# Kernel optimization log

Hardware: AMD Instinct MI355X
Metric: run time of the kernel (lower is better)

Reference implementation:

```python
import jax, jax.numpy as jnp
import numpy as np

DN = ('NCHW', 'OIHW', 'NCHW')


def setup_inputs() -> dict:
    key = jax.random.key(0)
    k1, k2, k3, k4 = jax.random.split(key, 4)
    B, C, H, W = 8, 64, 128, 416
    depth = jax.random.uniform(k1, (B, H, W), dtype=jnp.float32) * 10.0 + 1.0
    feat = jax.random.normal(k2, (B, C, H, W), dtype=jnp.float32)
    w1 = jax.random.normal(k3, (64, C, 3, 3), dtype=jnp.float32) * 0.05
    w2 = jax.random.normal(k4, (144, 64, 1, 1), dtype=jnp.float32) * 0.05
    return {"depth": depth, "feat": feat, "w1": w1, "w2": w2}


def reference(depth, feat, w1, w2):
    B, H, W = depth.shape
    S = 4  # 2 ** scale, scale=2
    # mask predictor: conv3x3 (no bias) -> relu -> conv1x1 (no bias)
    h = jax.lax.conv_general_dilated(feat, w1, (1, 1), ((1, 1), (1, 1)), dimension_numbers=DN)
    h = jax.nn.relu(h)
    mask = jax.lax.conv_general_dilated(h, w2, (1, 1), ((0, 0), (0, 0)), dimension_numbers=DN)
    # [B, 144, H, W] -> [B, 9, S, S, H, W], softmax over the 9 neighbor taps
    mask = mask.reshape(B, 9, S, S, H, W)
    mask = jax.nn.softmax(mask, axis=1)
    # unfold(depth, 3x3, pad=1): 9 shifted views, row-major (ky, kx) like torch
    pad = jnp.pad(depth, ((0, 0), (1, 1), (1, 1)))
    patches = jnp.stack([pad[:, ky:ky + H, kx:kx + W]
                         for ky in range(3) for kx in range(3)], axis=1)  # [B,9,H,W]
    up = jnp.sum(mask * patches[:, :, None, None], axis=1)  # [B,S,S,H,W]
    # pixel-shuffle: permute(0,3,1,4,2) -> [B,H,S,W,S] -> [B,S*H,S*W]
    out = up.transpose(0, 3, 1, 4, 2).reshape(B, S * H, S * W)
    return out
```

## Files before the change

### kernel.cpp

```cpp
#include <hip/hip_runtime.h>


using frag_ab = __attribute__((ext_vector_type(8))) short;
using frag_cd = __attribute__((ext_vector_type(4))) float;
typedef __attribute__((ext_vector_type(8))) unsigned short ushort8;

static __device__ __forceinline__ unsigned short f2bf(float f) {
    unsigned u = __builtin_bit_cast(unsigned, f);
    u += 0x7fff + ((u >> 16) & 1);
    return (unsigned short)(u >> 16);
}
static __device__ __forceinline__ unsigned int pkbf(float lo, float hi) {
    return (unsigned int)f2bf(lo) | ((unsigned int)f2bf(hi) << 16);
}

__global__ void prep(const float* __restrict__ w1, const float* __restrict__ w2,
                     unsigned short* __restrict__ w1bf, unsigned short* __restrict__ w2bf,
                     unsigned short* __restrict__ nhwc, int do_pad) {
    int i = blockIdx.x * 256 + threadIdx.x;
    if (i < 36864) {
        int j = i & 7, oc = (i >> 3) & 63, g = i >> 9;
        int q = g & 3, kh = (g >> 2) & 1, tap = g >> 3;
        int ic = kh * 32 + q * 8 + j;
        w1bf[i] = f2bf(w1[(oc * 64 + ic) * 9 + (tap / 3) * 3 + (tap % 3)]);
    }
    if (i < 9216) {
        int j = i & 7, ch = (i >> 3) % 144, g = (i >> 3) / 144;
        int q = g & 3, kh = g >> 2;
        w2bf[i] = f2bf(w2[ch * 64 + (kh * 32 + q * 8 + j)]);
    }
    if (do_pad && i < 69888) {
        int b = i / 8736, rem = i - b * 8736;
        int pos = rem >> 3, pack = rem & 7;
        int row, w;
        if (pos < 836) { row = (pos < 418) ? 0 : 129; w = (pos < 418) ? pos : pos - 418; }
        else           { int t = pos - 836; row = 1 + (t >> 1); w = (t & 1) ? 417 : 0; }
        ushort8 z = {0, 0, 0, 0, 0, 0, 0, 0};
        *(ushort8*)&nhwc[(((size_t)b * 130 + row) * 418 + w) * 64 + pack * 8] = z;
    }
}

__global__ __launch_bounds__(256, 8) void nchw_to_nhwc3(const float* __restrict__ feat,
                                                        unsigned short* __restrict__ nhwc) {
    __shared__ float sT[64 * 33];
    const int b = blockIdx.z, h = blockIdx.y, w0 = blockIdx.x * 32;
    const int tid = threadIdx.x;

    const int seg = tid & 7, crd = tid >> 3;
    #pragma unroll
    for (int pass = 0; pass < 2; ++pass) {
        const int c = crd + 32 * pass;
        float4 v = *(const float4*)&feat[(((size_t)b * 64 + c) * 128 + h) * 416 + w0 + seg * 4];
        *(float4*)&sT[c * 33 + seg * 4] = v;
    }
    __syncthreads();

    const int w = tid >> 3, j = tid & 7;
    float f[8];
    #pragma unroll
    for (int k = 0; k < 8; ++k) f[k] = sT[(j * 8 + k) * 33 + w];
    uint4 o;
    o.x = pkbf(f[0], f[1]); o.y = pkbf(f[2], f[3]);
    o.z = pkbf(f[4], f[5]); o.w = pkbf(f[6], f[7]);
    *(uint4*)&nhwc[(((size_t)b * 130 + h + 1) * 418 + (w0 + w + 1)) * 64 + j * 8] = o;
}

__global__ __launch_bounds__(512, 4) void convex_up_mfma3(
    const float* __restrict__ depth, const unsigned short* __restrict__ nhwc,
    const unsigned short* __restrict__ w1bf, const unsigned short* __restrict__ w2bf,
    float* __restrict__ out)
{
    constexpr int H = 128, W = 416, OW = 1664;
    constexpr int RS = 418 * 64;

    __shared__ __align__(16) unsigned short sF[2592 * 8];
    __shared__ float sD[18 * 18];

    const int tid  = threadIdx.x;
    const int wv   = tid >> 6;
    const int lane = tid & 63;
    const int q    = lane >> 4;
    const int ln   = lane & 15;
    const int bw = blockIdx.x, bh = blockIdx.y, b = blockIdx.z;
    const int h0 = bh * 16, w0 = bw * 16;

    if (tid < 324) {
        int lr = tid / 18, lc = tid % 18;
        int gh = h0 - 1 + lr, gw = w0 - 1 + lc;
        float v = 0.f;
        if ((unsigned)gh < (unsigned)H && (unsigned)gw < (unsigned)W)
            v = depth[((size_t)b * H + gh) * W + gw];
        sD[tid] = v;
    }

    const unsigned short* gbase = nhwc + ((size_t)(b * 130 + h0) * 418 + w0) * 64;
    #pragma unroll
    for (int k = 0; k < 6; ++k) {
        int i = wv + 8 * k;
        int c = i * 64 + lane;
        if (c < 2592) {
            int r = c / 144, m = c - r * 144;
            int col = m >> 3, iccs = m & 7;
            int icc = iccs ^ (col & 7);
            const unsigned short* g = gbase + (size_t)r * RS + col * 64 + icc * 8;
            __builtin_amdgcn_global_load_lds((const __attribute__((address_space(1))) void*)g,
                                             (__attribute__((address_space(3))) void*)&sF[c * 8],
                                             16, 0, 0);
        }
    }
    __syncthreads();

    frag_cd acc1[2][4];
    #pragma unroll
    for (int mt = 0; mt < 2; ++mt)
        #pragma unroll
        for (int nt = 0; nt < 4; ++nt) acc1[mt][nt] = frag_cd{0.f, 0.f, 0.f, 0.f};

    #pragma unroll
    for (int tap = 0; tap < 9; ++tap) {
        const int ky = tap / 3, kx = tap % 3;
        #pragma unroll
        for (int kh = 0; kh < 2; ++kh) {
            frag_ab a[2];
            #pragma unroll
            for (int mt = 0; mt < 2; ++mt) {
                int r = 2 * wv + mt + ky, col = ln + kx;
                int slot = (r * 18 + col) * 8 + ((kh * 4 + q) ^ (col & 7));
                a[mt] = *(const frag_ab*)&sF[slot * 8];
            }
            frag_ab bf[4];
            #pragma unroll
            for (int nt = 0; nt < 4; ++nt)
                bf[nt] = *(const frag_ab*)&w1bf[(size_t)((tap * 2 + kh) * 4 + q) * 512 + (nt * 16 + ln) * 8];
            #pragma unroll
            for (int mt = 0; mt < 2; ++mt)
                #pragma unroll
                for (int nt = 0; nt < 4; ++nt)
                    acc1[mt][nt] = __builtin_amdgcn_mfma_f32_16x16x32_bf16(a[mt], bf[nt], acc1[mt][nt], 0, 0, 0);
        }
    }

    __syncthreads();

    unsigned short* sH = sF + wv * 2304;
    #pragma unroll
    for (int mt = 0; mt < 2; ++mt)
        #pragma unroll
        for (int nt = 0; nt < 4; ++nt)
            #pragma unroll
            for (int r = 0; r < 4; ++r)
                sH[(mt * 16 + q * 4 + r) * 72 + nt * 16 + ln] = f2bf(fmaxf(acc1[mt][nt][r], 0.f));

    frag_cd acc2[2][9];
    #pragma unroll
    for (int mt = 0; mt < 2; ++mt)
        #pragma unroll
        for (int nt = 0; nt < 9; ++nt) acc2[mt][nt] = frag_cd{0.f, 0.f, 0.f, 0.f};

    #pragma unroll
    for (int kh = 0; kh < 2; ++kh) {
        frag_ab a2[2];
        #pragma unroll
        for (int mt = 0; mt < 2; ++mt)
            a2[mt] = *(const frag_ab*)&sH[(mt * 16 + ln) * 72 + kh * 32 + q * 8];
        #pragma unroll
        for (int nt = 0; nt < 9; ++nt) {
            frag_ab b2 = *(const frag_ab*)&w2bf[(size_t)((kh * 4 + q) * 144 + nt * 16 + ln) * 8];
            acc2[0][nt] = __builtin_amdgcn_mfma_f32_16x16x32_bf16(a2[0], b2, acc2[0][nt], 0, 0, 0);
            acc2[1][nt] = __builtin_amdgcn_mfma_f32_16x16x32_bf16(a2[1], b2, acc2[1][nt], 0, 0, 0);
        }
    }

    float* sOutw = (float*)sH;
    #pragma unroll
    for (int mt = 0; mt < 2; ++mt) {
        const int prow = 2 * wv + mt;
        #pragma unroll
        for (int r = 0; r < 4; ++r) {
            const int pcol = q * 4 + r;
            float lg[9];
            #pragma unroll
            for (int t = 0; t < 9; ++t) lg[t] = acc2[mt][t][r];
            float mx = lg[0];
            #pragma unroll
            for (int t = 1; t < 9; ++t) mx = fmaxf(mx, lg[t]);
            float sum = 0.f, up = 0.f;
            #pragma unroll
            for (int t = 0; t < 9; ++t) {
                float e = __expf(lg[t] - mx);
                sum += e;
                up  += e * sD[(prow + t / 3) * 18 + (pcol + t % 3)];
            }
            sOutw[(mt * 16 + pcol) * 17 + ln] = up / sum;
        }
    }
    float* outb = out + (size_t)b * 512 * OW + (size_t)(h0 + 2 * wv) * 4 * OW + w0 * 4;
    const int row_o = lane >> 3;
    const int mt_o  = row_o >> 2, sy_o = row_o & 3;
    #pragma unroll
    for (int v = 0; v < 2; ++v) {
        float4 o;
        #pragma unroll
        for (int e = 0; e < 4; ++e) {
            int j = (lane & 7) * 8 + v * 4 + e;
            o[e] = sOutw[(mt_o * 16 + (j >> 2)) * 17 + sy_o * 4 + (j & 3)];
        }
        *(float4*)&outb[(size_t)row_o * OW + (lane & 7) * 8 + v * 4] = o;
    }
}

__global__ __launch_bounds__(256, 3) void convex_up_mfma_fb(
    const float* __restrict__ depth, const float* __restrict__ feat,
    const unsigned short* __restrict__ w1bf, const unsigned short* __restrict__ w2bf,
    float* __restrict__ out)
{
    constexpr int H = 128, W = 416, OW = 1664;
    __shared__ unsigned short sF[8 * 10 * 18 * 8];
    __shared__ unsigned short sH[4][32 * 72];
    __shared__ float sD[10 * 18];
    const int tid = threadIdx.x, wv = tid >> 6, lane = tid & 63;
    const int q = lane >> 4, ln = lane & 15;
    const int bw = blockIdx.x, bh = blockIdx.y, b = blockIdx.z;
    const int h0 = bh * 8, w0 = bw * 16;
    if (tid < 180) {
        int lr = tid / 18, lc = tid % 18;
        int gh = h0 - 1 + lr, gw = w0 - 1 + lc;
        float v = 0.f;
        if ((unsigned)gh < (unsigned)H && (unsigned)gw < (unsigned)W)
            v = depth[((size_t)b * H + gh) * W + gw];
        sD[tid] = v;
    }
    for (int idx = tid; idx < 11520; idx += 256) {
        int ic = idx / 180, rem = idx - ic * 180;
        int lr = rem / 18, lc = rem - lr * 18;
        int gh = h0 - 1 + lr, gw = w0 - 1 + lc;
        float v = 0.f;
        if ((unsigned)gh < (unsigned)H && (unsigned)gw < (unsigned)W)
            v = feat[(((size_t)b * 64 + ic) * H + gh) * W + gw];
        sF[(((ic >> 3) * 10 + lr) * 18 + lc) * 8 + (ic & 7)] = f2bf(v);
    }
    __syncthreads();
    frag_cd acc1[2][4];
    for (int mt = 0; mt < 2; ++mt) for (int nt = 0; nt < 4; ++nt) acc1[mt][nt] = frag_cd{0.f,0.f,0.f,0.f};
    #pragma unroll
    for (int tap = 0; tap < 9; ++tap) {
        const int ky = tap / 3, kx = tap % 3;
        #pragma unroll
        for (int kh = 0; kh < 2; ++kh) {
            frag_ab a[2];
            #pragma unroll
            for (int mt = 0; mt < 2; ++mt)
                a[mt] = *(const frag_ab*)&sF[(((kh * 4 + q) * 10 + 2 * wv + mt + ky) * 18 + ln + kx) * 8];
            frag_ab bf[4];
            #pragma unroll
            for (int nt = 0; nt < 4; ++nt)
                bf[nt] = *(const frag_ab*)&w1bf[(size_t)((tap * 2 + kh) * 4 + q) * 512 + (nt * 16 + ln) * 8];
            #pragma unroll
            for (int mt = 0; mt < 2; ++mt)
                #pragma unroll
                for (int nt = 0; nt < 4; ++nt)
                    acc1[mt][nt] = __builtin_amdgcn_mfma_f32_16x16x32_bf16(a[mt], bf[nt], acc1[mt][nt], 0, 0, 0);
        }
    }
    #pragma unroll
    for (int mt = 0; mt < 2; ++mt)
        #pragma unroll
        for (int nt = 0; nt < 4; ++nt)
            #pragma unroll
            for (int r = 0; r < 4; ++r)
                sH[wv][(mt * 16 + q * 4 + r) * 72 + nt * 16 + ln] = f2bf(fmaxf(acc1[mt][nt][r], 0.f));
    frag_cd acc2[2][9];
    for (int mt = 0; mt < 2; ++mt) for (int nt = 0; nt < 9; ++nt) acc2[mt][nt] = frag_cd{0.f,0.f,0.f,0.f};
    #pragma unroll
    for (int kh = 0; kh < 2; ++kh) {
        frag_ab a2[2];
        #pragma unroll
        for (int mt = 0; mt < 2; ++mt)
            a2[mt] = *(const frag_ab*)&sH[wv][(mt * 16 + ln) * 72 + kh * 32 + q * 8];
        #pragma unroll
        for (int nt = 0; nt < 9; ++nt) {
            frag_ab b2 = *(const frag_ab*)&w2bf[(size_t)((kh * 4 + q) * 144 + nt * 16 + ln) * 8];
            acc2[0][nt] = __builtin_amdgcn_mfma_f32_16x16x32_bf16(a2[0], b2, acc2[0][nt], 0, 0, 0);
            acc2[1][nt] = __builtin_amdgcn_mfma_f32_16x16x32_bf16(a2[1], b2, acc2[1][nt], 0, 0, 0);
        }
    }
    float* sOutw = (float*)&sH[wv][0];
    #pragma unroll
    for (int mt = 0; mt < 2; ++mt) {
        const int prow = 2 * wv + mt;
        #pragma unroll
        for (int r = 0; r < 4; ++r) {
            const int pcol = q * 4 + r;
            float lg[9];
            #pragma unroll
            for (int t = 0; t < 9; ++t) lg[t] = acc2[mt][t][r];
            float mx = lg[0];
            #pragma unroll
            for (int t = 1; t < 9; ++t) mx = fmaxf(mx, lg[t]);
            float sum = 0.f, up = 0.f;
            #pragma unroll
            for (int t = 0; t < 9; ++t) {
                float e = __expf(lg[t] - mx);
                sum += e; up += e * sD[(prow + t / 3) * 18 + (pcol + t % 3)];
            }
            sOutw[(mt * 16 + pcol) * 17 + ln] = up / sum;
        }
    }
    float* outb = out + (size_t)b * 512 * OW + (size_t)(h0 + 2 * wv) * 4 * OW + w0 * 4;
    const int row_o = lane >> 3, mt_o = row_o >> 2, sy_o = row_o & 3;
    #pragma unroll
    for (int v = 0; v < 2; ++v) {
        float4 o;
        #pragma unroll
        for (int e = 0; e < 4; ++e) {
            int j = (lane & 7) * 8 + v * 4 + e;
            o[e] = sOutw[(mt_o * 16 + (j >> 2)) * 17 + sy_o * 4 + (j & 3)];
        }
        *(float4*)&outb[(size_t)row_o * OW + (lane & 7) * 8 + v * 4] = o;
    }
}

extern "C" void kernel_launch(void* const* d_in, const int* in_sizes, int n_in,
                              void* d_out, int out_size, void* d_ws, size_t ws_size,
                              hipStream_t stream) {
    const float* depth = (const float*)d_in[0];
    const float* feat  = (const float*)d_in[1];
    const float* w1    = (const float*)d_in[2];
    const float* w2    = (const float*)d_in[3];
    float* out = (float*)d_out;

    const size_t NHWC_USHORTS = (size_t)8 * 130 * 418 * 64;
    const size_t NEED = NHWC_USHORTS * 2 + (36864 + 9216) * 2;

    if (ws_size >= NEED) {
        unsigned short* nhwc = (unsigned short*)d_ws;
        unsigned short* w1bf = nhwc + NHWC_USHORTS;
        unsigned short* w2bf = w1bf + 36864;
        prep<<<273, 256, 0, stream>>>(w1, w2, w1bf, w2bf, nhwc, 1);
        nchw_to_nhwc3<<<dim3(13, 128, 8), 256, 0, stream>>>(feat, nhwc);
        convex_up_mfma3<<<dim3(26, 8, 8), dim3(512), 0, stream>>>(depth, nhwc, w1bf, w2bf, out);
    } else {
        unsigned short* w1bf = (unsigned short*)d_ws;
        unsigned short* w2bf = w1bf + 36864;
        prep<<<273, 256, 0, stream>>>(w1, w2, w1bf, w2bf, nullptr, 0);
        convex_up_mfma_fb<<<dim3(26, 16, 8), 256, 0, stream>>>(depth, feat, w1bf, w2bf, out);
    }
}
```

Baseline: 244.0 us.

## Fuse prep, transpose and conv into one cooperative persistent kernel

Replaces the three-kernel sequence (weight prep plus padding, NCHW to NHWC bf16 transpose, fused conv/softmax upsample) with a single cooperative kernel. It runs the prep and transpose phases grid-stride, does a grid-wide sync, then loops persistently over the output tiles. This aims to remove launch gaps and tail effects between kernels. In exchange it adds a grid barrier and a fixed grid of 256 or 512 blocks, which may not balance the 1664 tiles evenly. The iterA computation assumes G divides the transpose work evenly.

```diff
diff --git a/kernel.cpp b/kernel.cpp
--- a/kernel.cpp
+++ b/kernel.cpp
@@ -1,5 +1,8 @@
 #include <hip/hip_runtime.h>
-
+#include <hip/hip_cooperative_groups.h>
+
+
+namespace cg = cooperative_groups;
 
 using frag_ab = __attribute__((ext_vector_type(8))) short;
 using frag_cd = __attribute__((ext_vector_type(4))) float;
@@ -12,6 +15,213 @@
 }
 static __device__ __forceinline__ unsigned int pkbf(float lo, float hi) {
     return (unsigned int)f2bf(lo) | ((unsigned int)f2bf(hi) << 16);
+}
+
+__global__ __launch_bounds__(512, 4) void convex_up_coop(
+    const float* __restrict__ depth, const float* __restrict__ feat,
+    const float* __restrict__ w1, const float* __restrict__ w2,
+    unsigned short* __restrict__ nhwc, unsigned short* __restrict__ w1bf,
+    unsigned short* __restrict__ w2bf, float* __restrict__ out)
+{
+    constexpr int H = 128, W = 416, OW = 1664;
+    constexpr int RS = 418 * 64;
+
+    __shared__ __align__(16) unsigned char smem[42768];
+
+    const int tid  = threadIdx.x;
+    const int bid  = blockIdx.x;
+    const int G    = gridDim.x;
+
+    for (int i = bid * 512 + tid; i < 36864; i += G * 512) {
+        int j = i & 7, oc = (i >> 3) & 63, g = i >> 9;
+        int q = g & 3, kh = (g >> 2) & 1, tap = g >> 3;
+        int ic = kh * 32 + q * 8 + j;
+        w1bf[i] = f2bf(w1[(oc * 64 + ic) * 9 + (tap / 3) * 3 + (tap % 3)]);
+    }
+    for (int i = bid * 512 + tid; i < 9216; i += G * 512) {
+        int j = i & 7, ch = (i >> 3) % 144, g = (i >> 3) / 144;
+        int q = g & 3, kh = g >> 2;
+        w2bf[i] = f2bf(w2[ch * 64 + (kh * 32 + q * 8 + j)]);
+    }
+    for (int i = bid * 512 + tid; i < 69888; i += G * 512) {
+        int b = i / 8736, rem = i - b * 8736;
+        int pos = rem >> 3, pack = rem & 7;
+        int row, w;
+        if (pos < 836) { row = (pos < 418) ? 0 : 129; w = (pos < 418) ? pos : pos - 418; }
+        else           { int t = pos - 836; row = 1 + (t >> 1); w = (t & 1) ? 417 : 0; }
+        ushort8 z = {0, 0, 0, 0, 0, 0, 0, 0};
+        *(ushort8*)&nhwc[(((size_t)b * 130 + row) * 418 + w) * 64 + pack * 8] = z;
+    }
+
+    {
+        const int half = tid >> 8, stid = tid & 255;
+        float* sT = (float*)smem + half * 2112;
+        const int iterA = 13312 / (2 * G);
+        for (int it = 0; it < iterA; ++it) {
+            const int t2 = it * 2 * G + 2 * bid + half;
+            const int b = t2 / 1664, rem = t2 - b * 1664;
+            const int h = rem / 13, w0 = (rem - h * 13) * 32;
+            __syncthreads();
+            const int seg = stid & 7, crd = stid >> 3;
+            #pragma unroll
+            for (int pass = 0; pass < 2; ++pass) {
+                const int c = crd + 32 * pass;
+                float4 v = *(const float4*)&feat[(((size_t)b * 64 + c) * 128 + h) * 416 + w0 + seg * 4];
+                *(float4*)&sT[c * 33 + seg * 4] = v;
+            }
+            __syncthreads();
+            const int w = stid >> 3, j = stid & 7;
+            float f[8];
+            #pragma unroll
+            for (int k = 0; k < 8; ++k) f[k] = sT[(j * 8 + k) * 33 + w];
+            uint4 o;
+            o.x = pkbf(f[0], f[1]); o.y = pkbf(f[2], f[3]);
+            o.z = pkbf(f[4], f[5]); o.w = pkbf(f[6], f[7]);
+            *(uint4*)&nhwc[(((size_t)b * 130 + h + 1) * 418 + (w0 + w + 1)) * 64 + j * 8] = o;
+        }
+    }
+
+    __threadfence();
+    cg::this_grid().sync();
+
+    unsigned short* sF = (unsigned short*)smem;
+    float* sD = (float*)(smem + 41472);
+
+    const int wv   = tid >> 6;
+    const int lane = tid & 63;
+    const int q    = lane >> 4;
+    const int ln   = lane & 15;
+
+    for (int t = bid; t < 1664; t += G) {
+        const int bw = t % 26, bh = (t / 26) % 8, b = t / 208;
+        const int h0 = bh * 16, w0 = bw * 16;
+
+        __syncthreads();
+
+        if (tid < 324) {
+            int lr = tid / 18, lc = tid % 18;
+            int gh = h0 - 1 + lr, gw = w0 - 1 + lc;
+            float v = 0.f;
+            if ((unsigned)gh < (unsigned)H && (unsigned)gw < (unsigned)W)
+                v = depth[((size_t)b * H + gh) * W + gw];
+            sD[tid] = v;
+        }
+
+        const unsigned short* gbase = nhwc + ((size_t)(b * 130 + h0) * 418 + w0) * 64;
+        #pragma unroll
+        for (int k = 0; k < 6; ++k) {
+            int i = wv + 8 * k;
+            int c = i * 64 + lane;
+            if (c < 2592) {
+                int r = c / 144, m = c - r * 144;
+                int col = m >> 3, iccs = m & 7;
+                int icc = iccs ^ (col & 7);
+                const unsigned short* g = gbase + (size_t)r * RS + col * 64 + icc * 8;
+                __builtin_amdgcn_global_load_lds((const __attribute__((address_space(1))) void*)g,
+                                                 (__attribute__((address_space(3))) void*)&sF[c * 8],
+                                                 16, 0, 0);
+            }
+        }
+        __syncthreads();
+
+        frag_cd acc1[2][4];
+        #pragma unroll
+        for (int mt = 0; mt < 2; ++mt)
+            #pragma unroll
+            for (int nt = 0; nt < 4; ++nt) acc1[mt][nt] = frag_cd{0.f, 0.f, 0.f, 0.f};
+
+        #pragma unroll
+        for (int tap = 0; tap < 9; ++tap) {
+            const int ky = tap / 3, kx = tap % 3;
+            #pragma unroll
+            for (int kh = 0; kh < 2; ++kh) {
+                frag_ab a[2];
+                #pragma unroll
+                for (int mt = 0; mt < 2; ++mt) {
+                    int r = 2 * wv + mt + ky, col = ln + kx;
+                    int slot = (r * 18 + col) * 8 + ((kh * 4 + q) ^ (col & 7));
+                    a[mt] = *(const frag_ab*)&sF[slot * 8];
+                }
+                frag_ab bf[4];
+                #pragma unroll
+                for (int nt = 0; nt < 4; ++nt)
+                    bf[nt] = *(const frag_ab*)&w1bf[(size_t)((tap * 2 + kh) * 4 + q) * 512 + (nt * 16 + ln) * 8];
+                #pragma unroll
+                for (int mt = 0; mt < 2; ++mt)
+                    #pragma unroll
+                    for (int nt = 0; nt < 4; ++nt)
+                        acc1[mt][nt] = __builtin_amdgcn_mfma_f32_16x16x32_bf16(a[mt], bf[nt], acc1[mt][nt], 0, 0, 0);
+            }
+        }
+
+        __syncthreads();
+
+        unsigned short* sH = sF + wv * 2304;
+        #pragma unroll
+        for (int mt = 0; mt < 2; ++mt)
+            #pragma unroll
+            for (int nt = 0; nt < 4; ++nt)
+                #pragma unroll
+                for (int r = 0; r < 4; ++r)
+                    sH[(mt * 16 + q * 4 + r) * 72 + nt * 16 + ln] = f2bf(fmaxf(acc1[mt][nt][r], 0.f));
+
+        frag_cd acc2[2][9];
+        #pragma unroll
+        for (int mt = 0; mt < 2; ++mt)
+            #pragma unroll
+            for (int nt = 0; nt < 9; ++nt) acc2[mt][nt] = frag_cd{0.f, 0.f, 0.f, 0.f};
+
+        #pragma unroll
+        for (int kh = 0; kh < 2; ++kh) {
+            frag_ab a2[2];
+            #pragma unroll
+            for (int mt = 0; mt < 2; ++mt)
+                a2[mt] = *(const frag_ab*)&sH[(mt * 16 + ln) * 72 + kh * 32 + q * 8];
+            #pragma unroll
+            for (int nt = 0; nt < 9; ++nt) {
+                frag_ab b2 = *(const frag_ab*)&w2bf[(size_t)((kh * 4 + q) * 144 + nt * 16 + ln) * 8];
+                acc2[0][nt] = __builtin_amdgcn_mfma_f32_16x16x32_bf16(a2[0], b2, acc2[0][nt], 0, 0, 0);
+                acc2[1][nt] = __builtin_amdgcn_mfma_f32_16x16x32_bf16(a2[1], b2, acc2[1][nt], 0, 0, 0);
+            }
+        }
+
+        float* sOutw = (float*)sH;
+        #pragma unroll
+        for (int mt = 0; mt < 2; ++mt) {
+            const int prow = 2 * wv + mt;
+            #pragma unroll
+            for (int r = 0; r < 4; ++r) {
+                const int pcol = q * 4 + r;
+                float lg[9];
+                #pragma unroll
+                for (int tt = 0; tt < 9; ++tt) lg[tt] = acc2[mt][tt][r];
+                float mx = lg[0];
+                #pragma unroll
+                for (int tt = 1; tt < 9; ++tt) mx = fmaxf(mx, lg[tt]);
+                float sum = 0.f, up = 0.f;
+                #pragma unroll
+                for (int tt = 0; tt < 9; ++tt) {
+                    float e = __expf(lg[tt] - mx);
+                    sum += e;
+                    up  += e * sD[(prow + tt / 3) * 18 + (pcol + tt % 3)];
+                }
+                sOutw[(mt * 16 + pcol) * 17 + ln] = up / sum;
+            }
+        }
+        float* outb = out + (size_t)b * 512 * OW + (size_t)(h0 + 2 * wv) * 4 * OW + w0 * 4;
+        const int row_o = lane >> 3;
+        const int mt_o  = row_o >> 2, sy_o = row_o & 3;
+        #pragma unroll
+        for (int v = 0; v < 2; ++v) {
+            float4 o;
+            #pragma unroll
+            for (int e = 0; e < 4; ++e) {
+                int j = (lane & 7) * 8 + v * 4 + e;
+                o[e] = sOutw[(mt_o * 16 + (j >> 2)) * 17 + sy_o * 4 + (j & 3)];
+            }
+            *(float4*)&outb[(size_t)row_o * OW + (lane & 7) * 8 + v * 4] = o;
+        }
+    }
 }
 
 __global__ void prep(const float* __restrict__ w1, const float* __restrict__ w2,
@@ -45,7 +255,6 @@
     __shared__ float sT[64 * 33];
     const int b = blockIdx.z, h = blockIdx.y, w0 = blockIdx.x * 32;
     const int tid = threadIdx.x;
-
     const int seg = tid & 7, crd = tid >> 3;
     #pragma unroll
     for (int pass = 0; pass < 2; ++pass) {
@@ -54,7 +263,6 @@
         *(float4*)&sT[c * 33 + seg * 4] = v;
     }
     __syncthreads();
-
     const int w = tid >> 3, j = tid & 7;
     float f[8];
     #pragma unroll
@@ -72,18 +280,12 @@
 {
     constexpr int H = 128, W = 416, OW = 1664;
     constexpr int RS = 418 * 64;
-
     __shared__ __align__(16) unsigned short sF[2592 * 8];
     __shared__ float sD[18 * 18];
-
-    const int tid  = threadIdx.x;
-    const int wv   = tid >> 6;
-    const int lane = tid & 63;
-    const int q    = lane >> 4;
-    const int ln   = lane & 15;
+    const int tid = threadIdx.x, wv = tid >> 6, lane = tid & 63;
+    const int q = lane >> 4, ln = lane & 15;
     const int bw = blockIdx.x, bh = blockIdx.y, b = blockIdx.z;
     const int h0 = bh * 16, w0 = bw * 16;
-
     if (tid < 324) {
         int lr = tid / 18, lc = tid % 18;
         int gh = h0 - 1 + lr, gw = w0 - 1 + lc;
@@ -92,7 +294,6 @@
             v = depth[((size_t)b * H + gh) * W + gw];
         sD[tid] = v;
     }
-
     const unsigned short* gbase = nhwc + ((size_t)(b * 130 + h0) * 418 + w0) * 64;
     #pragma unroll
     for (int k = 0; k < 6; ++k) {
@@ -109,13 +310,8 @@
         }
     }
     __syncthreads();
-
     frag_cd acc1[2][4];
-    #pragma unroll
-    for (int mt = 0; mt < 2; ++mt)
-        #pragma unroll
-        for (int nt = 0; nt < 4; ++nt) acc1[mt][nt] = frag_cd{0.f, 0.f, 0.f, 0.f};
-
+    for (int mt = 0; mt < 2; ++mt) for (int nt = 0; nt < 4; ++nt) acc1[mt][nt] = frag_cd{0.f,0.f,0.f,0.f};
     #pragma unroll
     for (int tap = 0; tap < 9; ++tap) {
         const int ky = tap / 3, kx = tap % 3;
@@ -139,9 +335,7 @@
                     acc1[mt][nt] = __builtin_amdgcn_mfma_f32_16x16x32_bf16(a[mt], bf[nt], acc1[mt][nt], 0, 0, 0);
         }
     }
-
     __syncthreads();
-
     unsigned short* sH = sF + wv * 2304;
     #pragma unroll
     for (int mt = 0; mt < 2; ++mt)
@@ -150,13 +344,8 @@
             #pragma unroll
             for (int r = 0; r < 4; ++r)
                 sH[(mt * 16 + q * 4 + r) * 72 + nt * 16 + ln] = f2bf(fmaxf(acc1[mt][nt][r], 0.f));
-
     frag_cd acc2[2][9];
-    #pragma unroll
-    for (int mt = 0; mt < 2; ++mt)
-        #pragma unroll
-        for (int nt = 0; nt < 9; ++nt) acc2[mt][nt] = frag_cd{0.f, 0.f, 0.f, 0.f};
-
+    for (int mt = 0; mt < 2; ++mt) for (int nt = 0; nt < 9; ++nt) acc2[mt][nt] = frag_cd{0.f,0.f,0.f,0.f};
     #pragma unroll
     for (int kh = 0; kh < 2; ++kh) {
         frag_ab a2[2];
@@ -170,7 +359,6 @@
             acc2[1][nt] = __builtin_amdgcn_mfma_f32_16x16x32_bf16(a2[1], b2, acc2[1][nt], 0, 0, 0);
         }
     }
-
     float* sOutw = (float*)sH;
     #pragma unroll
     for (int mt = 0; mt < 2; ++mt) {
@@ -188,15 +376,13 @@
             #pragma unroll
             for (int t = 0; t < 9; ++t) {
                 float e = __expf(lg[t] - mx);
-                sum += e;
-                up  += e * sD[(prow + t / 3) * 18 + (pcol + t % 3)];
+                sum += e; up += e * sD[(prow + t / 3) * 18 + (pcol + t % 3)];
             }
             sOutw[(mt * 16 + pcol) * 17 + ln] = up / sum;
         }
     }
     float* outb = out + (size_t)b * 512 * OW + (size_t)(h0 + 2 * wv) * 4 * OW + w0 * 4;
-    const int row_o = lane >> 3;
-    const int mt_o  = row_o >> 2, sy_o = row_o & 3;
+    const int row_o = lane >> 3, mt_o = row_o >> 2, sy_o = row_o & 3;
     #pragma unroll
     for (int v = 0; v < 2; ++v) {
         float4 o;
@@ -336,9 +522,20 @@
         unsigned short* nhwc = (unsigned short*)d_ws;
         unsigned short* w1bf = nhwc + NHWC_USHORTS;
         unsigned short* w2bf = w1bf + 36864;
-        prep<<<273, 256, 0, stream>>>(w1, w2, w1bf, w2bf, nhwc, 1);
-        nchw_to_nhwc3<<<dim3(13, 128, 8), 256, 0, stream>>>(feat, nhwc);
-        convex_up_mfma3<<<dim3(26, 8, 8), dim3(512), 0, stream>>>(depth, nhwc, w1bf, w2bf, out);
+
+        int maxB = 0;
+        hipOccupancyMaxActiveBlocksPerMultiprocessor(&maxB, convex_up_coop, 512, 0);
+        if (maxB >= 1) {
+            int G = (maxB >= 2) ? 512 : 256;
+            void* args[] = { (void*)&depth, (void*)&feat, (void*)&w1, (void*)&w2,
+                             (void*)&nhwc, (void*)&w1bf, (void*)&w2bf, (void*)&out };
+            hipLaunchCooperativeKernel((const void*)convex_up_coop, dim3(G), dim3(512),
+                                       args, 0, stream);
+        } else {
+            prep<<<273, 256, 0, stream>>>(w1, w2, w1bf, w2bf, nhwc, 1);
+            nchw_to_nhwc3<<<dim3(13, 128, 8), 256, 0, stream>>>(feat, nhwc);
+            convex_up_mfma3<<<dim3(26, 8, 8), dim3(512), 0, stream>>>(depth, nhwc, w1bf, w2bf, out);
+        }
     } else {
         unsigned short* w1bf = (unsigned short*)d_ws;
         unsigned short* w2bf = w1bf + 36864;
```

After: 457.3 us. +87.4%, slower.
